# Optimization experiments

Hardware: AMD Instinct MI355X
Metric: run time of the kernel (lower is better)

## Reference

```python
import jax, jax.numpy as jnp
import numpy as np

EMB = 1024
HEADS = 16
EPS = 1e-6


def setup_inputs() -> dict:
    key = jax.random.key(0)
    ks = jax.random.split(key, 12)
    B, S, D = 2, 2048, EMB
    scale = 1.0 / np.sqrt(D)
    inp = {
        "v": jax.random.normal(ks[0], (B, S, D), jnp.float32),
        "k": jax.random.normal(ks[1], (B, S, D), jnp.float32),
        "q": jax.random.normal(ks[2], (B, S, D), jnp.float32),
        "Wv": jax.random.normal(ks[3], (D, D), jnp.float32) * scale,
        "bv": jnp.zeros((D,), jnp.float32),
        "Wk": jax.random.normal(ks[4], (D, D), jnp.float32) * scale,
        "bk": jnp.zeros((D,), jnp.float32),
        "Wq": jax.random.normal(ks[5], (D, D), jnp.float32) * scale,
        "bq": jnp.zeros((D,), jnp.float32),
        "Wo": jax.random.normal(ks[6], (D, D), jnp.float32) * scale,
        "bo": jnp.zeros((D,), jnp.float32),
        "gamma": jnp.ones((D,), jnp.float32),
        "beta": jnp.zeros((D,), jnp.float32),
    }
    return inp


def reference(v, k, q, Wv, bv, Wk, bk, Wq, bq, Wo, bo, gamma, beta):
    B, S, D = q.shape
    H = HEADS
    d = D // H  # head depth

    def split_heads(x):  # [B,S,D] -> [B,H,S,d]
        return x.reshape(B, S, H, d).transpose(0, 2, 1, 3)

    V = split_heads(v @ Wv + bv)
    K = split_heads(k @ Wk + bk)
    Q = split_heads(q @ Wq + bq)

    # scaled dot-product attention (full score matrix, no mask)
    scores = jnp.einsum("bhqd,bhkd->bhqk", Q, K) / jnp.sqrt(jnp.float32(d))
    attn = jax.nn.softmax(scores, axis=-1)
    ctx = jnp.einsum("bhqk,bhkd->bhqd", attn, V)

    ctx = ctx.transpose(0, 2, 1, 3).reshape(B, S, D)
    out = ctx @ Wo + bo + q  # final dense + residual

    # LayerNormalization(epsilon=1e-6) over last axis
    mu = jnp.mean(out, axis=-1, keepdims=True)
    var = jnp.var(out, axis=-1, keepdims=True)
    return gamma * (out - mu) * jax.lax.rsqrt(var + EPS) + beta
```

## Files before the change

### kernel.cpp

```cpp
#include <hip/hip_runtime.h>
#include <hip/hip_bf16.h>
#include <math.h>

#define D_EMB 1024
#define NBATCH 2
#define SEQ 2048
#define NH 16
#define HDIM 64
#define MTOT (NBATCH*SEQ)

typedef unsigned short u16;
typedef __attribute__((ext_vector_type(8))) short bf16x8;
typedef __attribute__((ext_vector_type(4))) float f32x4;
typedef __attribute__((ext_vector_type(16))) float f32x16;
typedef __attribute__((ext_vector_type(4))) unsigned short u16x4;
typedef __attribute__((ext_vector_type(4))) unsigned int u32x4;

__device__ __forceinline__ u16 f2b(float f) {
  union { float f; unsigned u; } x; x.f = f;
  unsigned r = x.u + 0x7fffu + ((x.u >> 16) & 1u);
  return (u16)(r >> 16);
}

__device__ __forceinline__ void gld_lds16(const u16* g, u16* l) {
  __builtin_amdgcn_global_load_lds(
      (const __attribute__((address_space(1))) void*)g,
      (__attribute__((address_space(3))) void*)l, 16, 0, 0);
}

__global__ __launch_bounds__(256) void convert_qkv(
    const float* __restrict__ v, const float* __restrict__ k, const float* __restrict__ q,
    u16* __restrict__ vb, u16* __restrict__ kb, u16* __restrict__ qb) {
  int idx = blockIdx.x * 256 + threadIdx.x;
  float4 a;
  u16x4 o;
  a = ((const float4*)v)[idx];
  o.x = f2b(a.x); o.y = f2b(a.y); o.z = f2b(a.z); o.w = f2b(a.w);
  ((u16x4*)vb)[idx] = o;
  a = ((const float4*)k)[idx];
  o.x = f2b(a.x); o.y = f2b(a.y); o.z = f2b(a.z); o.w = f2b(a.w);
  ((u16x4*)kb)[idx] = o;
  a = ((const float4*)q)[idx];
  o.x = f2b(a.x); o.y = f2b(a.y); o.z = f2b(a.z); o.w = f2b(a.w);
  ((u16x4*)qb)[idx] = o;
}

__global__ __launch_bounds__(256) void transpose_w(
    const float* __restrict__ Wv, const float* __restrict__ Wk,
    const float* __restrict__ Wq, const float* __restrict__ Wo,
    u16* __restrict__ Wvt, u16* __restrict__ Wkt,
    u16* __restrict__ Wqt, u16* __restrict__ Wot) {
  __shared__ float tile[32][33];
  int z = blockIdx.z;
  const float* W = (z==0) ? Wv : (z==1) ? Wk : (z==2) ? Wq : Wo;
  u16* Wt = (z==0) ? Wvt : (z==1) ? Wkt : (z==2) ? Wqt : Wot;
  int tx = threadIdx.x, ty = threadIdx.y;
  int n0 = blockIdx.x * 32, k0 = blockIdx.y * 32;
#pragma unroll
  for (int i = 0; i < 4; ++i)
    tile[ty + i*8][tx] = W[(size_t)(k0 + ty + i*8) * D_EMB + n0 + tx];
  __syncthreads();
#pragma unroll
  for (int i = 0; i < 4; ++i)
    Wt[(size_t)(n0 + ty + i*8) * D_EMB + k0 + tx] = f2b(tile[tx][ty + i*8]);
}

__device__ __forceinline__ void gemm_loop(
    const u16* __restrict__ A, const u16* __restrict__ Bt,
    u16* lds_a, u16* lds_b, int bm, int bn, int wid, int lane,
    int wr, int wc, f32x4 acc[4][4]) {
#pragma unroll 1
  for (int kt = 0; kt < D_EMB/64; ++kt) {
    __syncthreads();
#pragma unroll
    for (int i = 0; i < 4; ++i) {
      int chunk = i*4 + wid;
      int row = chunk*8 + (lane >> 3);
      int slot = (lane & 7) ^ (row & 7);
      const u16* srcA = A + (size_t)(bm*128 + row) * D_EMB + kt*64 + slot*8;
      gld_lds16(srcA, lds_a + chunk*512);
      const u16* srcB = Bt + (size_t)(bn*128 + row) * D_EMB + kt*64 + slot*8;
      gld_lds16(srcB, lds_b + chunk*512);
    }
    __syncthreads();
#pragma unroll
    for (int st = 0; st < 2; ++st) {
      bf16x8 af[4], bfr[4];
#pragma unroll
      for (int mb = 0; mb < 4; ++mb) {
        int row = wr*64 + mb*16 + (lane & 15);
        int slot = (st*4 + (lane >> 4)) ^ (row & 7);
        af[mb] = *(const bf16x8*)(lds_a + row*64 + slot*8);
      }
#pragma unroll
      for (int nb = 0; nb < 4; ++nb) {
        int row = wc*64 + nb*16 + (lane & 15);
        int slot = (st*4 + (lane >> 4)) ^ (row & 7);
        bfr[nb] = *(const bf16x8*)(lds_b + row*64 + slot*8);
      }
#pragma unroll
      for (int mb = 0; mb < 4; ++mb)
#pragma unroll
        for (int nb = 0; nb < 4; ++nb)
          acc[mb][nb] = __builtin_amdgcn_mfma_f32_16x16x32_bf16(af[mb], bfr[nb], acc[mb][nb], 0, 0, 0);
    }
  }
}

__global__ __launch_bounds__(256) void gemm_qkv(
    const u16* __restrict__ vb, const u16* __restrict__ kb, const u16* __restrict__ qb,
    const u16* __restrict__ Wvt, const u16* __restrict__ Wkt, const u16* __restrict__ Wqt,
    const float* __restrict__ bv, const float* __restrict__ bk, const float* __restrict__ bq,
    u16* __restrict__ Vt, u16* __restrict__ Kh, u16* __restrict__ Qh) {
  __shared__ u16 lds_a[128*64];
  __shared__ u16 lds_b[128*64];
  int z = blockIdx.z;
  const u16* A  = (z==0) ? vb : (z==1) ? kb : qb;
  const u16* Bt = (z==0) ? Wvt : (z==1) ? Wkt : Wqt;
  const float* bias = (z==0) ? bv : (z==1) ? bk : bq;
  int tid = threadIdx.x, wid = tid >> 6, lane = tid & 63;
  int wr = wid >> 1, wc = wid & 1;
  int bm = blockIdx.y, bn = blockIdx.x;
  f32x4 acc[4][4];
#pragma unroll
  for (int i = 0; i < 4; ++i)
#pragma unroll
    for (int j = 0; j < 4; ++j) acc[i][j] = (f32x4){0.f,0.f,0.f,0.f};
  gemm_loop(A, Bt, lds_a, lds_b, bm, bn, wid, lane, wr, wc, acc);
  int g = lane >> 4, c = lane & 15;
#pragma unroll
  for (int mb = 0; mb < 4; ++mb) {
    int row0 = bm*128 + wr*64 + mb*16 + g*4;
#pragma unroll
    for (int nb = 0; nb < 4; ++nb) {
      int col = bn*128 + wc*64 + nb*16 + c;
      float bsv = bias[col];
      int h = col >> 6, dd = col & 63;
      if (z == 2) {
#pragma unroll
        for (int r = 0; r < 4; ++r) {
          int m = row0 + r; int b = m >> 11, s = m & (SEQ-1);
          float val = (acc[mb][nb][r] + bsv) * 0.18033688f;
          Qh[(((size_t)b*NH + h)*SEQ + s)*HDIM + dd] = f2b(val);
        }
      } else if (z == 1) {
#pragma unroll
        for (int r = 0; r < 4; ++r) {
          int m = row0 + r; int b = m >> 11, s = m & (SEQ-1);
          Kh[(((size_t)b*NH + h)*SEQ + s)*HDIM + dd] = f2b(acc[mb][nb][r] + bsv);
        }
      } else {
        int m = row0; int b = m >> 11, s = m & (SEQ-1);
        u16x4 pk;
        pk.x = f2b(acc[mb][nb][0] + bsv);
        pk.y = f2b(acc[mb][nb][1] + bsv);
        pk.z = f2b(acc[mb][nb][2] + bsv);
        pk.w = f2b(acc[mb][nb][3] + bsv);
        *(u16x4*)(Vt + (((size_t)b*NH + h)*HDIM + dd)*SEQ + s) = pk;
      }
    }
  }
}

__global__ __launch_bounds__(256, 2) void attn_k(
    const u16* __restrict__ Qh, const u16* __restrict__ Kh,
    const u16* __restrict__ Vt, u16* __restrict__ ctx) {
  __shared__ u16 kt_lds[2][64*64];
  __shared__ u16 vt_lds[2][64*64];
  const int tid = threadIdx.x, wid = tid >> 6, lane = tid & 63;
  const int lo5 = lane & 31, hi = lane >> 5;
  const int bh = blockIdx.y;
  const int qb = blockIdx.x * 128 + wid * 32;
  const size_t base = (size_t)bh * SEQ * HDIM;

  const int srow = tid >> 3;
  const int sslot = (tid & 7) ^ (srow & 7);
  const u16* ksrc0 = Kh + base + (size_t)srow * HDIM + sslot*8;
  const u16* ksrc1 = Kh + base + (size_t)(srow+32) * HDIM + sslot*8;
  const u16* vsrc0 = Vt + base + (size_t)srow * SEQ + sslot*8;
  const u16* vsrc1 = Vt + base + (size_t)(srow+32) * SEQ + sslot*8;

  bf16x8 qf[4];
#pragma unroll
  for (int t = 0; t < 4; ++t)
    qf[t] = *(const bf16x8*)(Qh + base + (size_t)(qb + lo5)*HDIM + t*16 + hi*8);

  f32x16 o0, o1;
#pragma unroll
  for (int i = 0; i < 16; ++i) { o0[i] = 0.f; o1[i] = 0.f; }
  float m = -1e30f, l = 0.f;
  const float THR = 11.5f;

  gld_lds16(ksrc0, &kt_lds[0][wid*512]);
  gld_lds16(ksrc1, &kt_lds[0][2048 + wid*512]);
  gld_lds16(vsrc0, &vt_lds[0][wid*512]);
  gld_lds16(vsrc1, &vt_lds[0][2048 + wid*512]);
  asm volatile("s_waitcnt vmcnt(0)");
  __syncthreads();

  int buf = 0;
#pragma unroll 1
  for (int kv = 0; kv < SEQ/64; ++kv) {
    if (kv < SEQ/64 - 1) {
      const size_t ko = (size_t)(kv+1) * 64 * HDIM;
      const size_t vo = (size_t)(kv+1) * 64;
      gld_lds16(ksrc0 + ko, &kt_lds[buf^1][wid*512]);
      gld_lds16(ksrc1 + ko, &kt_lds[buf^1][2048 + wid*512]);
      gld_lds16(vsrc0 + vo, &vt_lds[buf^1][wid*512]);
      gld_lds16(vsrc1 + vo, &vt_lds[buf^1][2048 + wid*512]);
    }
    f32x16 st0, st1;
#pragma unroll
    for (int i = 0; i < 16; ++i) { st0[i] = 0.f; st1[i] = 0.f; }
    const int rsl = lo5 & 7;
#pragma unroll
    for (int t = 0; t < 4; ++t) {
      int slot = (2*t + hi) ^ rsl;
      bf16x8 kf0 = *(const bf16x8*)(&kt_lds[buf][lo5*64 + slot*8]);
      bf16x8 kf1 = *(const bf16x8*)(&kt_lds[buf][(32+lo5)*64 + slot*8]);
      st0 = __builtin_amdgcn_mfma_f32_32x32x16_bf16(kf0, qf[t], st0, 0, 0, 0);
      st1 = __builtin_amdgcn_mfma_f32_32x32x16_bf16(kf1, qf[t], st1, 0, 0, 0);
    }
    bf16x8 vf0[4], vf1[4];
#pragma unroll
    for (int t = 0; t < 4; ++t) {
      int slot = (2*t + hi) ^ rsl;
      vf0[t] = *(const bf16x8*)(&vt_lds[buf][lo5*64 + slot*8]);
      vf1[t] = *(const bf16x8*)(&vt_lds[buf][(32+lo5)*64 + slot*8]);
    }
    float pm = st0[0];
#pragma unroll
    for (int r = 1; r < 16; ++r) pm = fmaxf(pm, st0[r]);
#pragma unroll
    for (int r = 0; r < 16; ++r) pm = fmaxf(pm, st1[r]);
    pm = fmaxf(pm, __shfl_xor(pm, 32));
    if (__any(pm > m + THR)) {
      float mn = fmaxf(m, pm);
      float scl = exp2f(m - mn);
      m = mn; l *= scl;
#pragma unroll
      for (int r = 0; r < 16; ++r) {
        int crow = (r & 3) + 8*(r >> 2) + 4*hi;
        float sr = __int_as_float(
            __builtin_amdgcn_ds_bpermute(crow << 2, __float_as_int(scl)));
        o0[r] *= sr; o1[r] *= sr;
      }
    }
    float rs = 0.f;
#pragma unroll
    for (int r = 0; r < 16; ++r) { st0[r] = exp2f(st0[r] - m); rs += st0[r]; }
#pragma unroll
    for (int r = 0; r < 16; ++r) { st1[r] = exp2f(st1[r] - m); rs += st1[r]; }
    rs += __shfl_xor(rs, 32);
    l += rs;
    bf16x8 pa[4];
#pragma unroll
    for (int ks = 0; ks < 2; ++ks) {
      const f32x16& s = ks ? st1 : st0;
      unsigned X[8];
#pragma unroll
      for (int w = 0; w < 8; ++w) {
        float lo_f = s[2*w], hi_f = s[2*w + 1];
        asm("v_cvt_pk_bf16_f32 %0, %1, %2" : "=v"(X[w]) : "v"(lo_f), "v"(hi_f));
      }
      asm volatile("v_permlane32_swap_b32 %0, %1" : "+v"(X[0]), "+v"(X[2]));
      asm volatile("v_permlane32_swap_b32 %0, %1" : "+v"(X[1]), "+v"(X[3]));
      asm volatile("v_permlane32_swap_b32 %0, %1" : "+v"(X[4]), "+v"(X[6]));
      asm volatile("v_permlane32_swap_b32 %0, %1" : "+v"(X[5]), "+v"(X[7]));
      union { u32x4 u; bf16x8 b; } cva, cvb;
      cva.u = (u32x4){X[0], X[1], X[2], X[3]};
      cvb.u = (u32x4){X[4], X[5], X[6], X[7]};
      pa[2*ks]   = cva.b;
      pa[2*ks+1] = cvb.b;
    }
#pragma unroll
    for (int t = 0; t < 4; ++t) {
      o0 = __builtin_amdgcn_mfma_f32_32x32x16_bf16(pa[t], vf0[t], o0, 0, 0, 0);
      o1 = __builtin_amdgcn_mfma_f32_32x32x16_bf16(pa[t], vf1[t], o1, 0, 0, 0);
    }
    asm volatile("s_waitcnt vmcnt(0)");
    __syncthreads();
    buf ^= 1;
  }
  const int b = bh >> 4, h = bh & 15;
  float linv = 1.0f / l;
#pragma unroll
  for (int r = 0; r < 16; ++r) {
    int crow = (r & 3) + 8*(r >> 2) + 4*hi;
    float lr = __int_as_float(
        __builtin_amdgcn_ds_bpermute(crow << 2, __float_as_int(linv)));
    int s = qb + crow;
    u16* row = ctx + ((size_t)(b*SEQ + s))*D_EMB + h*64;
    row[lo5]      = f2b(o0[r] * lr);
    row[32 + lo5] = f2b(o1[r] * lr);
  }
}

__global__ __launch_bounds__(256) void gemm_out(
    const u16* __restrict__ ctx, const u16* __restrict__ Wot,
    const float* __restrict__ bo, const float* __restrict__ resid,
    float* __restrict__ preln) {
  __shared__ u16 lds_a[128*64];
  __shared__ u16 lds_b[128*64];
  int tid = threadIdx.x, wid = tid >> 6, lane = tid & 63;
  int wr = wid >> 1, wc = wid & 1;
  int bm = blockIdx.y, bn = blockIdx.x;
  f32x4 acc[4][4];
#pragma unroll
  for (int i = 0; i < 4; ++i)
#pragma unroll
    for (int j = 0; j < 4; ++j) acc[i][j] = (f32x4){0.f,0.f,0.f,0.f};
  gemm_loop(ctx, Wot, lds_a, lds_b, bm, bn, wid, lane, wr, wc, acc);
  int g = lane >> 4, c = lane & 15;
#pragma unroll
  for (int mb = 0; mb < 4; ++mb) {
    int row0 = bm*128 + wr*64 + mb*16 + g*4;
#pragma unroll
    for (int nb = 0; nb < 4; ++nb) {
      int col = bn*128 + wc*64 + nb*16 + c;
      float bsv = bo[col];
#pragma unroll
      for (int r = 0; r < 4; ++r) {
        int m = row0 + r;
        preln[(size_t)m*D_EMB + col] = acc[mb][nb][r] + bsv + resid[(size_t)m*D_EMB + col];
      }
    }
  }
}

__global__ __launch_bounds__(256) void ln_k(
    const float* __restrict__ preln, const float* __restrict__ gamma,
    const float* __restrict__ beta, float* __restrict__ out) {
  int row = blockIdx.x, tid = threadIdx.x;
  float4 x = ((const float4*)(preln + (size_t)row*D_EMB))[tid];
  float s  = x.x + x.y + x.z + x.w;
  float ss = x.x*x.x + x.y*x.y + x.z*x.z + x.w*x.w;
#pragma unroll
  for (int off = 32; off; off >>= 1) {
    s  += __shfl_xor(s, off);
    ss += __shfl_xor(ss, off);
  }
  __shared__ float red_s[4], red_ss[4];
  int wid = tid >> 6, lane = tid & 63;
  if (lane == 0) { red_s[wid] = s; red_ss[wid] = ss; }
  __syncthreads();
  s  = red_s[0] + red_s[1] + red_s[2] + red_s[3];
  ss = red_ss[0] + red_ss[1] + red_ss[2] + red_ss[3];
  float mu = s * (1.0f/1024.0f);
  float var = ss * (1.0f/1024.0f) - mu*mu;
  float rstd = rsqrtf(var + 1e-6f);
  float4 gm = ((const float4*)gamma)[tid];
  float4 bt = ((const float4*)beta)[tid];
  float4 y;
  y.x = (x.x - mu)*rstd*gm.x + bt.x;
  y.y = (x.y - mu)*rstd*gm.y + bt.y;
  y.z = (x.z - mu)*rstd*gm.z + bt.z;
  y.w = (x.w - mu)*rstd*gm.w + bt.w;
  ((float4*)(out + (size_t)row*D_EMB))[tid] = y;
}

extern "C" void kernel_launch(void* const* d_in, const int* in_sizes, int n_in,
                              void* d_out, int out_size, void* d_ws, size_t ws_size,
                              hipStream_t stream) {
  const float* v_in  = (const float*)d_in[0];
  const float* k_in  = (const float*)d_in[1];
  const float* q_in  = (const float*)d_in[2];
  const float* Wv    = (const float*)d_in[3];
  const float* bv    = (const float*)d_in[4];
  const float* Wk    = (const float*)d_in[5];
  const float* bk    = (const float*)d_in[6];
  const float* Wq    = (const float*)d_in[7];
  const float* bq    = (const float*)d_in[8];
  const float* Wo    = (const float*)d_in[9];
  const float* bo    = (const float*)d_in[10];
  const float* gamma = (const float*)d_in[11];
  const float* beta  = (const float*)d_in[12];
  char* ws = (char*)d_ws;

  const size_t TOKB = (size_t)MTOT * D_EMB * 2;
  const size_t WB   = (size_t)D_EMB * D_EMB * 2;
  size_t o_qb = 0;
  size_t o_kb = o_qb + TOKB;
  size_t o_vb = o_kb + TOKB;
  size_t o_wq = o_vb + TOKB;
  size_t o_wk = o_wq + WB;
  size_t o_wv = o_wk + WB;
  size_t o_wo = o_wv + WB;
  size_t o_Qh = o_wo + WB;
  size_t o_Kh = o_Qh + TOKB;
  size_t o_Vt = o_Kh + TOKB;
  size_t o_cx = o_Vt + TOKB;

  u16* qb  = (u16*)(ws + o_qb);
  u16* kb  = (u16*)(ws + o_kb);
  u16* vb  = (u16*)(ws + o_vb);
  u16* wqt = (u16*)(ws + o_wq);
  u16* wkt = (u16*)(ws + o_wk);
  u16* wvt = (u16*)(ws + o_wv);
  u16* wot = (u16*)(ws + o_wo);
  u16* Qh  = (u16*)(ws + o_Qh);
  u16* Kh  = (u16*)(ws + o_Kh);
  u16* Vt  = (u16*)(ws + o_Vt);
  u16* cx  = (u16*)(ws + o_cx);
  float* preln = (float*)(ws + 0);

  convert_qkv<<<4096, 256, 0, stream>>>(v_in, k_in, q_in, vb, kb, qb);
  transpose_w<<<dim3(32, 32, 4), dim3(32, 8), 0, stream>>>(Wv, Wk, Wq, Wo, wvt, wkt, wqt, wot);
  gemm_qkv<<<dim3(8, 32, 3), 256, 0, stream>>>(vb, kb, qb, wvt, wkt, wqt, bv, bk, bq, Vt, Kh, Qh);
  attn_k<<<dim3(16, 32), 256, 0, stream>>>(Qh, Kh, Vt, cx);
  gemm_out<<<dim3(8, 32), 256, 0, stream>>>(cx, wot, bo, q_in, preln);
  ln_k<<<4096, 256, 0, stream>>>(preln, gamma, beta, (float*)d_out);
}
```

Before: 164.6 us.

## Restructure attention inner loop with unrolled double buffer, MFMA row sums, new swizzle

Rewrites the flash-attention KV loop so the double-buffered stages are unrolled by two, with static LDS buffer offsets and precomputed fragment addresses. The LDS swizzle gains an extra XOR term to cut bank conflicts. The softmax row sum is now computed by extra MFMAs against a ones vector instead of VALU adds and shuffles. s_setprio is placed around the MFMA blocks. This trades four extra MFMAs per tile and more accumulator registers for less VALU and cross-lane work, and the sum now runs on bf16-rounded probabilities.

```diff
diff --git a/kernel.cpp b/kernel.cpp
--- a/kernel.cpp
+++ b/kernel.cpp
@@ -174,121 +174,139 @@
   const size_t base = (size_t)bh * SEQ * HDIM;
 
   const int srow = tid >> 3;
-  const int sslot = (tid & 7) ^ (srow & 7);
-  const u16* ksrc0 = Kh + base + (size_t)srow * HDIM + sslot*8;
-  const u16* ksrc1 = Kh + base + (size_t)(srow+32) * HDIM + sslot*8;
-  const u16* vsrc0 = Vt + base + (size_t)srow * SEQ + sslot*8;
-  const u16* vsrc1 = Vt + base + (size_t)(srow+32) * SEQ + sslot*8;
+  const int c0 = (tid & 7) ^ (srow & 7) ^ (srow >> 3);
+  const int c1 = c0 ^ 4;
+  const u16* kp0 = Kh + base + (size_t)srow * HDIM + c0*8;
+  const u16* kp1 = Kh + base + (size_t)(srow+32) * HDIM + c1*8;
+  const u16* vp0 = Vt + base + (size_t)srow * SEQ + c0*8;
+  const u16* vp1 = Vt + base + (size_t)(srow+32) * SEQ + c1*8;
+
+  const int r7 = lo5 & 7, r3 = lo5 >> 3;
+  int offs0[4], offs1[4];
+#pragma unroll
+  for (int t = 0; t < 4; ++t) {
+    int p = (2*t + hi) ^ r7 ^ r3;
+    offs0[t] = lo5*128 + p*16;
+    offs1[t] = (lo5+32)*128 + (p^4)*16;
+  }
+  const char* ktbase = (const char*)&kt_lds[0][0];
+  const char* vtbase = (const char*)&vt_lds[0][0];
 
   bf16x8 qf[4];
 #pragma unroll
   for (int t = 0; t < 4; ++t)
     qf[t] = *(const bf16x8*)(Qh + base + (size_t)(qb + lo5)*HDIM + t*16 + hi*8);
 
-  f32x16 o0, o1;
-#pragma unroll
-  for (int i = 0; i < 16; ++i) { o0[i] = 0.f; o1[i] = 0.f; }
-  float m = -1e30f, l = 0.f;
+  bf16x8 onesf;
+#pragma unroll
+  for (int j = 0; j < 8; ++j) onesf[j] = (short)0x3F80;
+  f32x16 z16;
+#pragma unroll
+  for (int i = 0; i < 16; ++i) z16[i] = 0.f;
+
+  f32x16 o0, o1, lacc;
+#pragma unroll
+  for (int i = 0; i < 16; ++i) { o0[i] = 0.f; o1[i] = 0.f; lacc[i] = 0.f; }
+  float m = -1e30f;
   const float THR = 11.5f;
 
-  gld_lds16(ksrc0, &kt_lds[0][wid*512]);
-  gld_lds16(ksrc1, &kt_lds[0][2048 + wid*512]);
-  gld_lds16(vsrc0, &vt_lds[0][wid*512]);
-  gld_lds16(vsrc1, &vt_lds[0][2048 + wid*512]);
+#define STAGE(B) do { \
+    gld_lds16(kp0, &kt_lds[B][wid*512]); \
+    gld_lds16(kp1, &kt_lds[B][2048 + wid*512]); \
+    gld_lds16(vp0, &vt_lds[B][wid*512]); \
+    gld_lds16(vp1, &vt_lds[B][2048 + wid*512]); \
+    kp0 += 64*HDIM; kp1 += 64*HDIM; vp0 += 64; vp1 += 64; \
+  } while (0)
+
+#define COMPUTE(B) do { \
+    const char* kb_ = ktbase + (B)*8192; \
+    const char* vb_ = vtbase + (B)*8192; \
+    bf16x8 kf0[4], kf1[4]; \
+    _Pragma("unroll") for (int t = 0; t < 4; ++t) { \
+      kf0[t] = *(const bf16x8*)(kb_ + offs0[t]); \
+      kf1[t] = *(const bf16x8*)(kb_ + offs1[t]); } \
+    __builtin_amdgcn_s_setprio(1); \
+    f32x16 st0 = __builtin_amdgcn_mfma_f32_32x32x16_bf16(kf0[0], qf[0], z16, 0, 0, 0); \
+    f32x16 st1 = __builtin_amdgcn_mfma_f32_32x32x16_bf16(kf1[0], qf[0], z16, 0, 0, 0); \
+    _Pragma("unroll") for (int t = 1; t < 4; ++t) { \
+      st0 = __builtin_amdgcn_mfma_f32_32x32x16_bf16(kf0[t], qf[t], st0, 0, 0, 0); \
+      st1 = __builtin_amdgcn_mfma_f32_32x32x16_bf16(kf1[t], qf[t], st1, 0, 0, 0); } \
+    __builtin_amdgcn_s_setprio(0); \
+    bf16x8 vf0[4], vf1[4]; \
+    _Pragma("unroll") for (int t = 0; t < 4; ++t) { \
+      vf0[t] = *(const bf16x8*)(vb_ + offs0[t]); \
+      vf1[t] = *(const bf16x8*)(vb_ + offs1[t]); } \
+    float pm = fmaxf(st0[0], st0[1]); \
+    _Pragma("unroll") for (int r = 2; r < 16; r += 2) \
+      pm = fmaxf(fmaxf(pm, st0[r]), st0[r+1]); \
+    _Pragma("unroll") for (int r = 0; r < 16; r += 2) \
+      pm = fmaxf(fmaxf(pm, st1[r]), st1[r+1]); \
+    pm = fmaxf(pm, __shfl_xor(pm, 32)); \
+    if (__any(pm > m + THR)) { \
+      float mn = fmaxf(m, pm); \
+      float scl = exp2f(m - mn); \
+      m = mn; \
+      _Pragma("unroll") for (int r = 0; r < 16; ++r) { \
+        int crow = (r & 3) + 8*(r >> 2) + 4*hi; \
+        float sr = __int_as_float( \
+            __builtin_amdgcn_ds_bpermute(crow << 2, __float_as_int(scl))); \
+        o0[r] *= sr; o1[r] *= sr; lacc[r] *= sr; } } \
+    _Pragma("unroll") for (int r = 0; r < 16; ++r) st0[r] = exp2f(st0[r] - m); \
+    _Pragma("unroll") for (int r = 0; r < 16; ++r) st1[r] = exp2f(st1[r] - m); \
+    bf16x8 pa[4]; \
+    _Pragma("unroll") for (int ks = 0; ks < 2; ++ks) { \
+      const f32x16& s_ = ks ? st1 : st0; \
+      unsigned X[8]; \
+      _Pragma("unroll") for (int w = 0; w < 8; ++w) { \
+        float lo_f = s_[2*w], hi_f = s_[2*w + 1]; \
+        asm("v_cvt_pk_bf16_f32 %0, %1, %2" : "=v"(X[w]) : "v"(lo_f), "v"(hi_f)); } \
+      asm volatile("v_permlane32_swap_b32 %0, %1" : "+v"(X[0]), "+v"(X[2])); \
+      asm volatile("v_permlane32_swap_b32 %0, %1" : "+v"(X[1]), "+v"(X[3])); \
+      asm volatile("v_permlane32_swap_b32 %0, %1" : "+v"(X[4]), "+v"(X[6])); \
+      asm volatile("v_permlane32_swap_b32 %0, %1" : "+v"(X[5]), "+v"(X[7])); \
+      union { u32x4 u; bf16x8 b; } cva, cvb; \
+      cva.u = (u32x4){X[0], X[1], X[2], X[3]}; \
+      cvb.u = (u32x4){X[4], X[5], X[6], X[7]}; \
+      pa[2*ks]   = cva.b; \
+      pa[2*ks+1] = cvb.b; } \
+    __builtin_amdgcn_s_setprio(1); \
+    _Pragma("unroll") for (int t = 0; t < 4; ++t) { \
+      o0 = __builtin_amdgcn_mfma_f32_32x32x16_bf16(pa[t], vf0[t], o0, 0, 0, 0); \
+      o1 = __builtin_amdgcn_mfma_f32_32x32x16_bf16(pa[t], vf1[t], o1, 0, 0, 0); } \
+    _Pragma("unroll") for (int t = 0; t < 4; ++t) \
+      lacc = __builtin_amdgcn_mfma_f32_32x32x16_bf16(pa[t], onesf, lacc, 0, 0, 0); \
+    __builtin_amdgcn_s_setprio(0); \
+  } while (0)
+
+  STAGE(0);
   asm volatile("s_waitcnt vmcnt(0)");
   __syncthreads();
 
-  int buf = 0;
 #pragma unroll 1
-  for (int kv = 0; kv < SEQ/64; ++kv) {
-    if (kv < SEQ/64 - 1) {
-      const size_t ko = (size_t)(kv+1) * 64 * HDIM;
-      const size_t vo = (size_t)(kv+1) * 64;
-      gld_lds16(ksrc0 + ko, &kt_lds[buf^1][wid*512]);
-      gld_lds16(ksrc1 + ko, &kt_lds[buf^1][2048 + wid*512]);
-      gld_lds16(vsrc0 + vo, &vt_lds[buf^1][wid*512]);
-      gld_lds16(vsrc1 + vo, &vt_lds[buf^1][2048 + wid*512]);
-    }
-    f32x16 st0, st1;
-#pragma unroll
-    for (int i = 0; i < 16; ++i) { st0[i] = 0.f; st1[i] = 0.f; }
-    const int rsl = lo5 & 7;
-#pragma unroll
-    for (int t = 0; t < 4; ++t) {
-      int slot = (2*t + hi) ^ rsl;
-      bf16x8 kf0 = *(const bf16x8*)(&kt_lds[buf][lo5*64 + slot*8]);
-      bf16x8 kf1 = *(const bf16x8*)(&kt_lds[buf][(32+lo5)*64 + slot*8]);
-      st0 = __builtin_amdgcn_mfma_f32_32x32x16_bf16(kf0, qf[t], st0, 0, 0, 0);
-      st1 = __builtin_amdgcn_mfma_f32_32x32x16_bf16(kf1, qf[t], st1, 0, 0, 0);
-    }
-    bf16x8 vf0[4], vf1[4];
-#pragma unroll
-    for (int t = 0; t < 4; ++t) {
-      int slot = (2*t + hi) ^ rsl;
-      vf0[t] = *(const bf16x8*)(&vt_lds[buf][lo5*64 + slot*8]);
-      vf1[t] = *(const bf16x8*)(&vt_lds[buf][(32+lo5)*64 + slot*8]);
-    }
-    float pm = st0[0];
-#pragma unroll
-    for (int r = 1; r < 16; ++r) pm = fmaxf(pm, st0[r]);
-#pragma unroll
-    for (int r = 0; r < 16; ++r) pm = fmaxf(pm, st1[r]);
-    pm = fmaxf(pm, __shfl_xor(pm, 32));
-    if (__any(pm > m + THR)) {
-      float mn = fmaxf(m, pm);
-      float scl = exp2f(m - mn);
-      m = mn; l *= scl;
-#pragma unroll
-      for (int r = 0; r < 16; ++r) {
-        int crow = (r & 3) + 8*(r >> 2) + 4*hi;
-        float sr = __int_as_float(
-            __builtin_amdgcn_ds_bpermute(crow << 2, __float_as_int(scl)));
-        o0[r] *= sr; o1[r] *= sr;
-      }
-    }
-    float rs = 0.f;
-#pragma unroll
-    for (int r = 0; r < 16; ++r) { st0[r] = exp2f(st0[r] - m); rs += st0[r]; }
-#pragma unroll
-    for (int r = 0; r < 16; ++r) { st1[r] = exp2f(st1[r] - m); rs += st1[r]; }
-    rs += __shfl_xor(rs, 32);
-    l += rs;
-    bf16x8 pa[4];
-#pragma unroll
-    for (int ks = 0; ks < 2; ++ks) {
-      const f32x16& s = ks ? st1 : st0;
-      unsigned X[8];
-#pragma unroll
-      for (int w = 0; w < 8; ++w) {
-        float lo_f = s[2*w], hi_f = s[2*w + 1];
-        asm("v_cvt_pk_bf16_f32 %0, %1, %2" : "=v"(X[w]) : "v"(lo_f), "v"(hi_f));
-      }
-      asm volatile("v_permlane32_swap_b32 %0, %1" : "+v"(X[0]), "+v"(X[2]));
-      asm volatile("v_permlane32_swap_b32 %0, %1" : "+v"(X[1]), "+v"(X[3]));
-      asm volatile("v_permlane32_swap_b32 %0, %1" : "+v"(X[4]), "+v"(X[6]));
-      asm volatile("v_permlane32_swap_b32 %0, %1" : "+v"(X[5]), "+v"(X[7]));
-      union { u32x4 u; bf16x8 b; } cva, cvb;
-      cva.u = (u32x4){X[0], X[1], X[2], X[3]};
-      cvb.u = (u32x4){X[4], X[5], X[6], X[7]};
-      pa[2*ks]   = cva.b;
-      pa[2*ks+1] = cvb.b;
-    }
-#pragma unroll
-    for (int t = 0; t < 4; ++t) {
-      o0 = __builtin_amdgcn_mfma_f32_32x32x16_bf16(pa[t], vf0[t], o0, 0, 0, 0);
-      o1 = __builtin_amdgcn_mfma_f32_32x32x16_bf16(pa[t], vf1[t], o1, 0, 0, 0);
-    }
+  for (int kv = 0; kv < SEQ/64 - 2; kv += 2) {
+    STAGE(1);
+    COMPUTE(0);
     asm volatile("s_waitcnt vmcnt(0)");
     __syncthreads();
-    buf ^= 1;
-  }
+    STAGE(0);
+    COMPUTE(1);
+    asm volatile("s_waitcnt vmcnt(0)");
+    __syncthreads();
+  }
+  STAGE(1);
+  COMPUTE(0);
+  asm volatile("s_waitcnt vmcnt(0)");
+  __syncthreads();
+  COMPUTE(1);
+
+#undef STAGE
+#undef COMPUTE
+
   const int b = bh >> 4, h = bh & 15;
-  float linv = 1.0f / l;
 #pragma unroll
   for (int r = 0; r < 16; ++r) {
     int crow = (r & 3) + 8*(r >> 2) + 4*hi;
-    float lr = __int_as_float(
-        __builtin_amdgcn_ds_bpermute(crow << 2, __float_as_int(linv)));
+    float lr = 1.0f / lacc[r];
     int s = qb + crow;
     u16* row = ctx + ((size_t)(b*SEQ + s))*D_EMB + h*64;
     row[lo5]      = f2b(o0[r] * lr);
```

Result: faster. 159.9 us (-2.9%).
